# Kernel tuning notes

Hardware: AMD Instinct MI355X
Metric: run time of the kernel (lower is better)

Reference implementation:

```python
import jax, jax.numpy as jnp
import numpy as np

R = 32            # voxel resolution
ALPHA = 0.1       # LeakyReLU slope
BN_EPS = 1e-4     # BatchNormalization epsilon
VOX_EPS = 1e-6    # Voxelization eps (normalize=True)


def _bn_train(x, gamma, beta, axes):
    # training-mode batch norm over `axes`, channel axis = 1
    mean = jnp.mean(x, axes, keepdims=True)
    var = jnp.var(x, axes, keepdims=True)
    bshape = (1, -1) + (1,) * (x.ndim - 2)
    return gamma.reshape(bshape) * (x - mean) * jax.lax.rsqrt(var + BN_EPS) + beta.reshape(bshape)


def _lrelu(x):
    return jnp.where(x >= 0, x, ALPHA * x)


def _voxelize(features, coords):
    # features [B,C,N], coords [B,3,N] -> grid [B,C,R,R,R], norm_coords [B,3,N] in [0,R-1]
    centered = coords - jnp.mean(coords, axis=2, keepdims=True)
    max_norm = jnp.max(jnp.linalg.norm(centered, axis=1, keepdims=True), axis=2, keepdims=True)
    norm = centered / (max_norm * 2.0 + VOX_EPS) + 0.5
    norm = jnp.clip(norm * R, 0.0, R - 1)
    vox = jnp.round(norm).astype(jnp.int32)              # [B,3,N]
    flat = (vox[:, 0] * R + vox[:, 1]) * R + vox[:, 2]   # [B,N]

    def per_batch(f, idx):  # f [C,N], idx [N]
        sums = jax.ops.segment_sum(f.T, idx, num_segments=R ** 3)            # [R^3,C]
        cnt = jax.ops.segment_sum(jnp.ones_like(idx, f.dtype), idx, num_segments=R ** 3)
        return (sums / jnp.maximum(cnt, 1.0)[:, None]).T                      # [C,R^3]

    grid = jax.vmap(per_batch)(features, flat)            # [B,C,R^3]
    B, C = features.shape[0], features.shape[1]
    return grid.reshape(B, C, R, R, R), norm


def _conv3d(x, w, b):
    # x [B,C,D,H,W], w [k,k,k,Cin,Cout], 'same' padding
    y = jax.lax.conv_general_dilated(x, w, (1, 1, 1), 'SAME',
                                     dimension_numbers=('NCDHW', 'DHWIO', 'NCDHW'))
    return y + b.reshape(1, -1, 1, 1, 1)


def _trilinear_devoxelize(vf, coords):
    # vf [B,C,R^3], coords [B,3,N] in [0,R-1] -> [B,C,N]
    c0f = jnp.clip(jnp.floor(coords), 0.0, R - 1)
    frac = coords - c0f                                   # [B,3,N]
    c0 = c0f.astype(jnp.int32)
    c1 = jnp.minimum(c0 + 1, R - 1)
    out = jnp.zeros((vf.shape[0], vf.shape[1], coords.shape[2]), vf.dtype)
    for dx in (0, 1):
        for dy in (0, 1):
            for dz in (0, 1):
                xs = c1[:, 0] if dx else c0[:, 0]
                ys = c1[:, 1] if dy else c0[:, 1]
                zs = c1[:, 2] if dz else c0[:, 2]
                w = ((frac[:, 0] if dx else 1 - frac[:, 0]) *
                     (frac[:, 1] if dy else 1 - frac[:, 1]) *
                     (frac[:, 2] if dz else 1 - frac[:, 2]))           # [B,N]
                idx = (xs * R + ys) * R + zs                            # [B,N]
                g = jnp.take_along_axis(vf, idx[:, None, :], axis=2)    # [B,C,N]
                out = out + w[:, None, :] * g
    return out


def setup_inputs() -> dict:
    key = jax.random.key(0)
    ks = jax.random.split(key, 16)
    B, C, N, K = 8, 64, 16384, 3
    s = 0.05
    return {
        'features': jax.random.normal(ks[0], (B, C, N), jnp.float32),
        'coords': jax.random.normal(ks[1], (B, 3, N), jnp.float32),
        'conv1_w': jax.random.normal(ks[2], (K, K, K, C, C), jnp.float32) * s,
        'conv1_b': jnp.zeros((C,), jnp.float32),
        'bn1_gamma': jnp.ones((C,), jnp.float32),
        'bn1_beta': jnp.zeros((C,), jnp.float32),
        'conv2_w': jax.random.normal(ks[3], (K, K, K, C, C), jnp.float32) * s,
        'conv2_b': jnp.zeros((C,), jnp.float32),
        'bn2_gamma': jnp.ones((C,), jnp.float32),
        'bn2_beta': jnp.zeros((C,), jnp.float32),
        'pf_w': jax.random.normal(ks[4], (C, C), jnp.float32) * s,
        'pf_bias': jnp.zeros((C,), jnp.float32),
        'pf_gamma': jnp.ones((C,), jnp.float32),
        'pf_beta': jnp.zeros((C,), jnp.float32),
    }


def reference(features, coords, conv1_w, conv1_b, bn1_gamma, bn1_beta,
              conv2_w, conv2_b, bn2_gamma, bn2_beta,
              pf_w, pf_bias, pf_gamma, pf_beta):
    vgrid, norm_coords = _voxelize(features, coords)
    v = _lrelu(_bn_train(_conv3d(vgrid, conv1_w, conv1_b), bn1_gamma, bn1_beta, (0, 2, 3, 4)))
    v = _lrelu(_bn_train(_conv3d(v, conv2_w, conv2_b), bn2_gamma, bn2_beta, (0, 2, 3, 4)))
    vflat = v.reshape(v.shape[0], v.shape[1], -1)                 # [B,C,R^3]
    vpts = _trilinear_devoxelize(vflat, norm_coords)              # [B,C,N]
    # point branch: shared MLP (1x1 conv) + BN + LeakyReLU
    p = jnp.einsum('bcn,cd->bdn', features, pf_w) + pf_bias[None, :, None]
    p = _lrelu(_bn_train(p, pf_gamma, pf_beta, (0, 2)))
    return vpts + p, coords
```

## Files before the change

kernel.cpp:

```cpp
#include <hip/hip_runtime.h>
#include <stdint.h>

#define RR 32
#define R3 32768
#define NB 8
#define NCH 64
#define NP 16384

typedef unsigned short u16;
typedef uint32_t u32;
typedef __attribute__((ext_vector_type(8))) short bf8;
typedef __attribute__((ext_vector_type(4))) float f4;
typedef __attribute__((ext_vector_type(16))) float f16x;

#define MFMA(a,b,c)   __builtin_amdgcn_mfma_f32_16x16x32_bf16(a,b,c,0,0,0)
#define MFMA32(a,b,c) __builtin_amdgcn_mfma_f32_32x32x16_bf16(a,b,c,0,0,0)

__device__ __forceinline__ float bf2f(u16 v){
  union { u32 u; float f; } x; x.u = ((u32)v) << 16; return x.f;
}
__device__ __forceinline__ float u2f(u32 u){
  union { u32 u; float f; } x; x.u = u; return x.f;
}
__device__ __forceinline__ u16 f2bf(float f){
  union { float f; u32 u; } x; x.f = f;
  u32 r = x.u + 0x7fffu + ((x.u >> 16) & 1u);
  return (u16)(r >> 16);
}
__device__ __forceinline__ float ldf(const void* p, size_t i, int isbf){
  return isbf ? bf2f(((const u16*)p)[i]) : ((const float*)p)[i];
}

#define OFF_GRID  0ull
#define OFF_BUF1  33554432ull
#define OFF_FT    33554432ull
#define OFF_P     67108864ull
#define OFF_CNT   83886080ull
#define OFF_SMALL 84934656ull
#define OFF_STAT  84936704ull
#define OFF_OFFS  84948992ull
#define OFF_NC    85997568ull
#define OFF_VIDX  87570432ull
#define OFF_SORT  88094720ull
#define OFF_WF1   88619008ull
#define OFF_WF2   88840192ull
#define OFF_WFP   89061376ull
#define WS_NEED   89069568ull
#define ZOFF      OFF_CNT
#define ZBYTES    1062912ull

__global__ void k_dtype(const uint32_t* __restrict__ gamma_raw, int* __restrict__ flag){
  if (threadIdx.x == 0) *flag = (gamma_raw[0] == 0x3F800000u) ? 0 : 1;
}

__global__ void k_coordstats(const void* __restrict__ coords, float* __restrict__ small,
                             const int* __restrict__ dflag){
  int b = blockIdx.x; int tid = threadIdx.x;
  int isbf = *dflag;
  __shared__ float red[1024];
  size_t cb = (size_t)b*3*NP;
  float sx=0.f, sy=0.f, sz=0.f;
  for (int n = tid; n < NP; n += 1024){
    sx += ldf(coords, cb+n, isbf);
    sy += ldf(coords, cb+NP+n, isbf);
    sz += ldf(coords, cb+2*NP+n, isbf);
  }
  float m[3]; float* sums[3] = {&sx,&sy,&sz};
  for (int a = 0; a < 3; a++){
    red[tid] = *sums[a]; __syncthreads();
    for (int s = 512; s > 0; s >>= 1){ if (tid < s) red[tid] += red[tid+s]; __syncthreads(); }
    m[a] = red[0] * (1.0f/NP); __syncthreads();
  }
  float vm = 0.f;
  for (int n = tid; n < NP; n += 1024){
    float cx = ldf(coords, cb+n, isbf)      - m[0];
    float cy = ldf(coords, cb+NP+n, isbf)   - m[1];
    float cz = ldf(coords, cb+2*NP+n, isbf) - m[2];
    vm = fmaxf(vm, sqrtf(cx*cx + cy*cy + cz*cz));
  }
  red[tid] = vm; __syncthreads();
  for (int s = 512; s > 0; s >>= 1){ if (tid < s) red[tid] = fmaxf(red[tid], red[tid+s]); __syncthreads(); }
  if (tid == 0){
    small[384 + b*4 + 0] = m[0];
    small[384 + b*4 + 1] = m[1];
    small[384 + b*4 + 2] = m[2];
    small[384 + b*4 + 3] = 1.0f / (2.0f*red[0] + 1e-6f);
  }
}

__global__ void k_pointprep(const void* __restrict__ coords, const float* __restrict__ small,
                            float* __restrict__ nc, int* __restrict__ vidx, int* __restrict__ cnt,
                            const int* __restrict__ dflag){
  int g = blockIdx.x*256 + threadIdx.x;
  int isbf = *dflag;
  int b = g >> 14; int n = g & (NP-1);
  float mx = small[384+b*4+0], my = small[384+b*4+1], mz = small[384+b*4+2], sc = small[384+b*4+3];
  size_t cb = (size_t)b*3*NP;
  float nx = ((ldf(coords, cb+n, isbf)      - mx)*sc + 0.5f) * 32.0f;
  float ny = ((ldf(coords, cb+NP+n, isbf)   - my)*sc + 0.5f) * 32.0f;
  float nz = ((ldf(coords, cb+2*NP+n, isbf) - mz)*sc + 0.5f) * 32.0f;
  nx = fminf(fmaxf(nx, 0.f), 31.f);
  ny = fminf(fmaxf(ny, 0.f), 31.f);
  nz = fminf(fmaxf(nz, 0.f), 31.f);
  nc[(b*3+0)*NP + n] = nx; nc[(b*3+1)*NP + n] = ny; nc[(b*3+2)*NP + n] = nz;
  int vx = (int)rintf(nx), vy = (int)rintf(ny), vz = (int)rintf(nz);
  int flat = (vx*32 + vy)*32 + vz;
  vidx[g] = flat;
  atomicAdd(&cnt[b*R3 + flat], 1);
}

__global__ void k_scan(const int* __restrict__ cnt, int* __restrict__ off){
  __shared__ int part[1024];
  int b = blockIdx.x, tid = threadIdx.x;
  int base = b*R3 + tid*32;
  int s = 0;
  for (int i = 0; i < 32; i++) s += cnt[base + i];
  part[tid] = s; __syncthreads();
  for (int st = 1; st < 1024; st <<= 1){
    int v = (tid >= st) ? part[tid - st] : 0;
    __syncthreads();
    part[tid] += v;
    __syncthreads();
  }
  int run = (tid == 0) ? 0 : part[tid - 1];
  for (int i = 0; i < 32; i++){ off[base + i] = run; run += cnt[base + i]; }
}

__global__ void k_sortpts(const int* __restrict__ vidx, int* __restrict__ off, int* __restrict__ sorted){
  int g = blockIdx.x*256 + threadIdx.x;
  int b = g >> 14; int n = g & (NP-1);
  int v = vidx[g];
  int slot = atomicAdd(&off[b*R3 + v], 1);
  sorted[b*NP + slot] = n;
}

__global__ __launch_bounds__(256) void k_voxsum(const u16* __restrict__ fT, const int* __restrict__ sorted,
                         const int* __restrict__ cnt, const int* __restrict__ off,
                         u16* __restrict__ grid){
  int wid = blockIdx.x*4 + (threadIdx.x >> 6);
  int lane = threadIdx.x & 63;
  int b = wid >> 11;
  int v0 = (wid & 2047) << 4;
  int base = b*R3 + v0;
  int c = 0, e = 0;
  if (lane < 16){ c = cnt[base + lane]; e = off[base + lane]; }
  int start = __shfl(e - c, 0);
  int total = __shfl(e, 15) - start;
  const int* sb = sorted + (size_t)b*NP;
  int sp = 0;
  if (lane < total) sp = sb[start + lane];
  #pragma unroll
  for (int i = 0; i < 16; i++){
    int ci = __shfl(c, i);
    int rel = __shfl(e, i) - ci - start;
    float a0 = 0.f, a1 = 0.f;
    int j = 0;
    for (; j + 1 < ci; j += 2){
      int k0 = rel + j, k1 = k0 + 1;
      int n0 = (k0 < 64) ? __shfl(sp, k0) : sb[start + k0];
      int n1 = (k1 < 64) ? __shfl(sp, k1) : sb[start + k1];
      a0 += bf2f(fT[((size_t)(b*NP + n0))*64 + lane]);
      a1 += bf2f(fT[((size_t)(b*NP + n1))*64 + lane]);
    }
    if (j < ci){
      int k0 = rel + j;
      int n0 = (k0 < 64) ? __shfl(sp, k0) : sb[start + k0];
      a0 += bf2f(fT[((size_t)(b*NP + n0))*64 + lane]);
    }
    float acc = a0 + a1;
    grid[((size_t)(base + i))*64 + lane] = f2bf(acc / (float)max(ci, 1));
  }
}

__global__ void k_wprep(const void* __restrict__ w, u16* __restrict__ wfrag, const int* __restrict__ dflag){
  int idx = blockIdx.x; int lane = threadIdx.x;
  int isbf = *dflag;
  int ntl = idx & 3; int kk = (idx >> 2) & 1; int tap = idx >> 3;
  int lh = lane & 15, quad = lane >> 4;
  int n = ntl*16 + lh;
  u16* dst = wfrag + ((size_t)idx*64 + lane)*8;
  for (int j = 0; j < 8; j++){
    int k = kk*32 + quad*8 + j;
    dst[j] = f2bf(ldf(w, (size_t)(tap*64 + k)*64 + n, isbf));
  }
}

__global__ void k_wprep32(const void* __restrict__ w, u16* __restrict__ wfrag, const int* __restrict__ dflag){
  int idx = blockIdx.x; int lane = threadIdx.x;
  int isbf = *dflag;
  int nh = idx & 1; int ks = (idx >> 1) & 3; int tap = idx >> 3;
  int n = nh*32 + (lane & 31);
  int khalf = lane >> 5;
  u16* dst = wfrag + ((size_t)idx*64 + lane)*8;
  for (int j = 0; j < 8; j++){
    int cin = ks*16 + khalf*8 + j;
    dst[j] = f2bf(ldf(w, (size_t)(tap*64 + cin)*64 + n, isbf));
  }
}

__device__ __forceinline__ void bn_params(const float* __restrict__ spread, int c, float invM,
                                          float* mean, float* rs){
  float su = 0.f, sq = 0.f;
  #pragma unroll
  for (int i = 0; i < 8; i++){ su += spread[i*128 + c]; sq += spread[i*128 + 64 + c]; }
  float m = su * invM;
  *mean = m;
  *rs = rsqrtf(sq*invM - m*m + 1e-4f);
}

#define ISSUE_W8(BANK, TAP) do { \
  _Pragma("unroll") \
  for (int k_ = 0; k_ < 8; k_++) \
    BANK[k_] = *(const bf8*)(wstream + (size_t)((TAP)*8 + k_)*512); \
} while(0)

#define ISSUE_A4(B0, TAP) do { \
  const int t_ = (TAP); \
  const int dwi_ = t_ % 3, dvi_ = (t_/3) % 3, dui_ = t_/9; \
  const u16* rp_ = &lds_in[((dui_ + usel)*4 + vsel + dvi_)*2176]; \
  const int wp_ = mlane + dwi_; \
  const int wb_ = wp_*64, wx_ = wp_ & 7; \
  _Pragma("unroll") \
  for (int ks_ = 0; ks_ < 4; ks_++){ \
    const int off_ = wb_ + ((((ks_*2) + khalf) ^ wx_) << 3); \
    B0[ks_] = *(const bf8*)(rp_ + off_); \
  } \
} while(0)

#define CONSUME(BW, B0) do { \
  _Pragma("unroll") \
  for (int ks_ = 0; ks_ < 4; ks_++){ \
    acc0 = MFMA32(B0[ks_], BW[ks_*2+0], acc0); \
    acc1 = MFMA32(B0[ks_], BW[ks_*2+1], acc1); \
  } \
} while(0)

template<int BN>
__global__ __launch_bounds__(256, 2) void k_conv_t(const u16* __restrict__ in, const u16* __restrict__ wfrag,
                                                   u16* __restrict__ out, const float* __restrict__ spread,
                                                   const void* __restrict__ gamma, const void* __restrict__ beta,
                                                   const int* __restrict__ dflag){
  __shared__ u16 lds_in[16*2176];
  __shared__ float bnA[64], bnB[64];
  int bx = blockIdx.x;
  int b = bx >> 8; int r = bx & 255;
  int u0 = (r >> 4) * 2; int v0 = (r & 15) * 2;
  int tid = threadIdx.x, wv = tid >> 6, lane = tid & 63;

  if constexpr (BN){
    if (tid < 64){
      int isbf = *dflag;
      float mean, rs;
      bn_params(spread, tid, 1.0f/(NB*R3), &mean, &rs);
      float ga = ldf(gamma, tid, isbf), be = ldf(beta, tid, isbf);
      float A = ga*rs;
      bnA[tid] = A; bnB[tid] = be - mean*A;
    }
    __syncthreads();
  }

  uint4 zz; zz.x = 0; zz.y = 0; zz.z = 0; zz.w = 0;
  for (int ri = wv; ri < 16; ri += 4){
    int u2 = u0 + (ri >> 2) - 1;
    int v2 = v0 + (ri & 3) - 1;
    uint4* dstrow = (uint4*)&lds_in[ri*2176];
    if ((unsigned)u2 > 31u || (unsigned)v2 > 31u){
      for (int i = lane; i < 272; i += 64) dstrow[i] = zz;
      continue;
    }
    const uint4* src = (const uint4*)(in + ((size_t)(b*R3 + (u2*32 + v2)*32))*64);
    if (lane < 8) dstrow[lane] = zz;
    else if (lane < 16) dstrow[264 + (lane & 7)] = zz;
    #pragma unroll
    for (int ch = 0; ch < 4; ch++){
      int idx = ch*64 + lane;
      int w = idx >> 3, cc = idx & 7;
      uint4 v = src[idx];
      if constexpr (BN){
        u32 in4[4] = {v.x, v.y, v.z, v.w};
        u32 o4[4];
        #pragma unroll
        for (int k = 0; k < 4; k++){
          int c = cc*8 + 2*k;
          float lo = u2f(in4[k] << 16);
          float hi = u2f(in4[k] & 0xFFFF0000u);
          lo = bnA[c]*lo + bnB[c];     lo = (lo >= 0.f) ? lo : 0.1f*lo;
          hi = bnA[c+1]*hi + bnB[c+1]; hi = (hi >= 0.f) ? hi : 0.1f*hi;
          o4[k] = (u32)f2bf(lo) | ((u32)f2bf(hi) << 16);
        }
        v.x = o4[0]; v.y = o4[1]; v.z = o4[2]; v.w = o4[3];
      }
      int wp = w + 1;
      dstrow[wp*8 + (cc ^ (wp & 7))] = v;
    }
  }
  __syncthreads();

  int usel = wv >> 1, vsel = wv & 1;
  int u_i = u0 + usel, v_i = v0 + vsel;
  int mlane = lane & 31;
  int khalf = lane >> 5;
  f16x acc0, acc1;
  #pragma unroll
  for (int i = 0; i < 16; i++){ acc0[i] = 0.f; acc1[i] = 0.f; }

  const u16* wstream = wfrag + (size_t)lane*8;

  bf8 W0[8], W1[8], W2[8];
  bf8 Aa[4], Ab[4];

  ISSUE_W8(W0, 0);
  ISSUE_W8(W1, 1);
  ISSUE_A4(Aa, 0);

  #pragma unroll
  for (int tap = 0; tap < 27; ++tap){
    const int pf = tap + 2;
    if (pf < 27){
      if (pf % 3 == 0)      ISSUE_W8(W0, pf);
      else if (pf % 3 == 1) ISSUE_W8(W1, pf);
      else                  ISSUE_W8(W2, pf);
    }
    if (tap + 1 < 27){
      if ((tap + 1) & 1) ISSUE_A4(Ab, tap + 1);
      else               ISSUE_A4(Aa, tap + 1);
    }
    __builtin_amdgcn_sched_barrier(0);
    if (tap < 25)       asm volatile("s_waitcnt vmcnt(16) lgkmcnt(4)");
    else if (tap == 25) asm volatile("s_waitcnt vmcnt(8) lgkmcnt(4)");
    else                asm volatile("s_waitcnt vmcnt(0) lgkmcnt(0)");
    __builtin_amdgcn_sched_barrier(0);
    const int wsel = tap % 3, asel = tap & 1;
    if (wsel == 0){ if (asel == 0) CONSUME(W0, Aa); else CONSUME(W0, Ab); }
    else if (wsel == 1){ if (asel == 0) CONSUME(W1, Aa); else CONSUME(W1, Ab); }
    else              { if (asel == 0) CONSUME(W2, Aa); else CONSUME(W2, Ab); }
  }

  int rbase = 4*khalf;
  size_t base0 = ((size_t)(b*R3 + (u_i*32 + v_i)*32))*64;
  #pragma unroll
  for (int reg = 0; reg < 16; reg++){
    int row = (reg & 3) + 8*(reg >> 2) + rbase;
    out[base0 + (size_t)row*64 + mlane]      = f2bf(acc0[reg]);
    out[base0 + (size_t)row*64 + 32 + mlane] = f2bf(acc1[reg]);
  }
}

__global__ __launch_bounds__(256) void k_stats2(const u16* __restrict__ buf, float* __restrict__ spread, int M){
  __shared__ float sred[4*128];
  int tid = threadIdx.x, bx = blockIdx.x;
  int wv = tid >> 6, lane = tid & 63;
  int sub = lane & 7;
  int g = bx*256 + tid;
  float s[8], s2[8];
  #pragma unroll
  for (int j = 0; j < 8; j++){ s[j] = 0.f; s2[j] = 0.f; }
  const uint4* p4 = (const uint4*)buf;
  size_t total = (size_t)M * 8;
  for (size_t f = g; f < total; f += 262144){
    uint4 v = p4[f];
    u32 ws_[4] = {v.x, v.y, v.z, v.w};
    #pragma unroll
    for (int k = 0; k < 4; k++){
      float lo = u2f(ws_[k] << 16);
      float hi = u2f(ws_[k] & 0xFFFF0000u);
      s[2*k]   += lo; s2[2*k]   += lo*lo;
      s[2*k+1] += hi; s2[2*k+1] += hi*hi;
    }
  }
  #pragma unroll
  for (int j = 0; j < 8; j++){
    #pragma unroll
    for (int m = 8; m <= 32; m <<= 1){
      s[j]  += __shfl_xor(s[j],  m);
      s2[j] += __shfl_xor(s2[j], m);
    }
  }
  if (lane < 8){
    #pragma unroll
    for (int j = 0; j < 8; j++){
      sred[wv*128 + sub*8 + j]      = s[j];
      sred[wv*128 + 64 + sub*8 + j] = s2[j];
    }
  }
  __syncthreads();
  if (tid < 128){
    float t = sred[tid] + sred[128+tid] + sred[256+tid] + sred[384+tid];
    atomicAdd(&spread[(bx & 7)*128 + tid], t);
  }
}

__global__ void k_ftrans(const void* __restrict__ feat, u16* __restrict__ fT, const int* __restrict__ dflag){
  __shared__ u16 t[64*65];
  int bx = blockIdx.x;
  int isbf = *dflag;
  int b = bx >> 8; int n0 = (bx & 255) * 64;
  int tid = threadIdx.x;
  int nl = tid & 63; int cq = tid >> 6;
  for (int cp = 0; cp < 16; cp++){
    int c = cq + cp*4;
    t[c*65 + nl] = f2bf(ldf(feat, ((size_t)(b*NCH + c))*NP + n0 + nl, isbf));
  }
  __syncthreads();
  for (int np2 = 0; np2 < 16; np2++){
    int n = np2*4 + cq; int c = nl;
    fT[((size_t)(b*NP + n0 + n))*64 + c] = t[c*65 + n];
  }
}

__global__ void k_pgemm(const u16* __restrict__ fT, const u16* __restrict__ wfp, u16* __restrict__ p){
  __shared__ u16 As[128*64];
  int bx = blockIdx.x;
  size_t row0 = (size_t)bx * 128;
  int tid = threadIdx.x, wv = tid >> 6, lane = tid & 63;
  const uint4* src = (const uint4*)(fT + row0*64);
  uint4* dst = (uint4*)As;
  for (int i = tid; i < 1024; i += 256) dst[i] = src[i];
  __syncthreads();
  int lh = lane & 15, quad = lane >> 4;
  f4 z4 = {0.f,0.f,0.f,0.f};
  f4 acc[2][4];
  for (int i = 0; i < 2; i++) for (int j = 0; j < 4; j++) acc[i][j] = z4;
  const u16* ap = &As[(wv*32)*64];
  #pragma unroll
  for (int kk = 0; kk < 2; kk++){
    bf8 a0 = *(const bf8*)(ap + lh*64 + kk*32 + quad*8);
    bf8 a1 = *(const bf8*)(ap + (16+lh)*64 + kk*32 + quad*8);
    #pragma unroll
    for (int ntl = 0; ntl < 4; ntl++){
      bf8 bf = *(const bf8*)(wfp + ((size_t)(kk*4 + ntl)*64 + lane)*8);
      acc[0][ntl] = MFMA(a0, bf, acc[0][ntl]);
      acc[1][ntl] = MFMA(a1, bf, acc[1][ntl]);
    }
  }
  #pragma unroll
  for (int mt = 0; mt < 2; mt++)
    for (int ntl = 0; ntl < 4; ntl++)
      for (int reg = 0; reg < 4; reg++){
        int rr = wv*32 + mt*16 + quad*4 + reg;
        p[(row0 + rr)*64 + ntl*16 + lh] = f2bf(acc[mt][ntl][reg]);
      }
}

__global__ void k_devox(const u16* __restrict__ grid, const u16* __restrict__ p,
                        const float* __restrict__ stP, const float* __restrict__ st2,
                        const void* __restrict__ pfg, const void* __restrict__ pfb,
                        const void* __restrict__ g2, const void* __restrict__ b2,
                        const float* __restrict__ nc, void* __restrict__ out0,
                        const int* __restrict__ dflag){
  __shared__ float t[64*65];
  int bx = blockIdx.x;
  int isbf = *dflag;
  int b = bx >> 8; int n0 = (bx & 255) * 64;
  int tid = threadIdx.x, wv = tid >> 6, lane = tid & 63;
  int c = lane;
  float meanP, rsP;
  bn_params(stP, c, 1.0f/(NB*NP), &meanP, &rsP);
  float gaP = ldf(pfg, c, isbf), beP = ldf(pfb, c, isbf);
  float mean2, rs2;
  bn_params(st2, c, 1.0f/(NB*R3), &mean2, &rs2);
  float ga2 = ldf(g2, c, isbf), be2 = ldf(b2, c, isbf);
  float A2 = ga2*rs2, B2 = be2 - mean2*A2;
  for (int pt = wv; pt < 64; pt += 4){
    int n = n0 + pt;
    float nx = nc[(b*3+0)*NP + n];
    float ny = nc[(b*3+1)*NP + n];
    float nz = nc[(b*3+2)*NP + n];
    float x0f = floorf(nx), y0f = floorf(ny), z0f = floorf(nz);
    int x0 = (int)x0f, y0 = (int)y0f, z0 = (int)z0f;
    float fx = nx - x0f, fy = ny - y0f, fz = nz - z0f;
    int x1 = min(x0+1,31), y1 = min(y0+1,31), z1 = min(z0+1,31);
    float acc = 0.f;
    #pragma unroll
    for (int k = 0; k < 8; k++){
      int dx = k >> 2, dy = (k >> 1) & 1, dz = k & 1;
      int xs = dx ? x1 : x0, ys = dy ? y1 : y0, zs = dz ? z1 : z0;
      float wgt = (dx ? fx : 1.f-fx)*(dy ? fy : 1.f-fy)*(dz ? fz : 1.f-fz);
      float gv = bf2f(grid[((size_t)(b*R3 + (xs*32+ys)*32 + zs))*64 + c]);
      gv = A2*gv + B2;
      gv = (gv >= 0.f) ? gv : 0.1f*gv;
      acc += wgt * gv;
    }
    float pv = bf2f(p[((size_t)(b*NP + n))*64 + c]);
    float y = gaP*(pv - meanP)*rsP + beP;
    y = (y >= 0.f) ? y : 0.1f*y;
    t[pt*65 + c] = acc + y;
  }
  __syncthreads();
  for (int cp = 0; cp < 16; cp++){
    int co = wv + cp*4;
    size_t oi = ((size_t)(b*NCH + co))*NP + n0 + lane;
    float val = t[lane*65 + co];
    if (isbf) ((u16*)out0)[oi] = f2bf(val);
    else      ((float*)out0)[oi] = val;
  }
}

__global__ void k_copycoords(const void* __restrict__ coords, void* __restrict__ out0,
                             const int* __restrict__ dflag){
  int g = blockIdx.x*256 + threadIdx.x;
  int isbf = *dflag;
  size_t oi = (size_t)NB*NCH*NP + g;
  if (isbf) ((u16*)out0)[oi]   = ((const u16*)coords)[g];
  else      ((float*)out0)[oi] = ((const float*)coords)[g];
}

extern "C" void kernel_launch(void* const* d_in, const int* in_sizes, int n_in,
                              void* d_out, int out_size, void* d_ws, size_t ws_size,
                              hipStream_t stream){
  if (ws_size < WS_NEED) return;

  const void* feat   = d_in[0];
  const void* coords = d_in[1];
  const void* w1     = d_in[2];
  const void* g1     = d_in[4];
  const void* b1     = d_in[5];
  const void* w2     = d_in[6];
  const void* g2     = d_in[8];
  const void* b2     = d_in[9];
  const void* pw     = d_in[10];
  const void* pg     = d_in[12];
  const void* pb     = d_in[13];

  char* ws = (char*)d_ws;
  u16*   gridv = (u16*)(ws + OFF_GRID);
  u16*   buf1  = (u16*)(ws + OFF_BUF1);
  u16*   fT    = (u16*)(ws + OFF_FT);
  u16*   p     = (u16*)(ws + OFF_P);
  int*   cnt   = (int*)(ws + OFF_CNT);
  float* small = (float*)(ws + OFF_SMALL);
  int*   dflag = (int*)(small + 448);
  float* stat  = (float*)(ws + OFF_STAT);
  int*   offs  = (int*)(ws + OFF_OFFS);
  float* nc    = (float*)(ws + OFF_NC);
  int*   vidx  = (int*)(ws + OFF_VIDX);
  int*   sorted= (int*)(ws + OFF_SORT);
  u16*   wf1   = (u16*)(ws + OFF_WF1);
  u16*   wf2   = (u16*)(ws + OFF_WF2);
  u16*   wfp   = (u16*)(ws + OFF_WFP);

  hipMemsetAsync(ws + ZOFF, 0, ZBYTES, stream);
  k_dtype<<<1, 64, 0, stream>>>((const uint32_t*)g1, dflag);

  k_wprep32<<<27*8, 64, 0, stream>>>(w1, wf1, dflag);
  k_wprep32<<<27*8, 64, 0, stream>>>(w2, wf2, dflag);
  k_wprep<<<8, 64, 0, stream>>>(pw, wfp, dflag);

  k_coordstats<<<NB, 1024, 0, stream>>>(coords, small, dflag);
  k_pointprep<<<NB*NP/256, 256, 0, stream>>>(coords, small, nc, vidx, cnt, dflag);
  k_scan<<<NB, 1024, 0, stream>>>(cnt, offs);
  k_sortpts<<<NB*NP/256, 256, 0, stream>>>(vidx, offs, sorted);

  k_ftrans<<<NB*NP/64, 256, 0, stream>>>(feat, fT, dflag);
  k_voxsum<<<NB*R3/64, 256, 0, stream>>>(fT, sorted, cnt, offs, gridv);
  k_pgemm<<<NB*NP/128, 256, 0, stream>>>(fT, wfp, p);
  k_stats2<<<1024, 256, 0, stream>>>(p, stat + 2048, NB*NP);

  k_conv_t<0><<<NB*256, 256, 0, stream>>>(gridv, wf1, buf1, nullptr, nullptr, nullptr, nullptr);
  k_stats2<<<1024, 256, 0, stream>>>(buf1, stat + 0, NB*R3);

  k_conv_t<1><<<NB*256, 256, 0, stream>>>(buf1, wf2, gridv, stat + 0, g1, b1, dflag);
  k_stats2<<<1024, 256, 0, stream>>>(gridv, stat + 1024, NB*R3);

  k_devox<<<NB*NP/64, 256, 0, stream>>>(gridv, p, stat + 2048, stat + 1024,
                                        pg, pb, g2, b2, nc, d_out, dflag);
  k_copycoords<<<NB*3*NP/256, 256, 0, stream>>>(coords, d_out, dflag);
}
```

Measured before the change: 421.4 us.

## Enlarge conv3d tile to 4x4 rows per block with 2 rows per wave

Each conv block now covers a 4x4 set of (u,v) rows using 8 waves, and each wave computes two u-rows. Every weight fragment loaded from global memory therefore feeds twice as many MFMAs, and the halo overhead in LDS shrinks from 16 staged rows per 4 outputs to 36 per 16. The cost is higher register pressure (four 16-float accumulators plus doubled A fragments), a larger LDS footprint (about 157 KB), and only 512 blocks total, which may reduce occupancy.

```diff
diff --git a/kernel.cpp b/kernel.cpp
--- a/kernel.cpp
+++ b/kernel.cpp
@@ -210,41 +210,45 @@
 
 #define ISSUE_W8(BANK, TAP) do { \
   _Pragma("unroll") \
-  for (int k_ = 0; k_ < 8; k_++) \
-    BANK[k_] = *(const bf8*)(wstream + (size_t)((TAP)*8 + k_)*512); \
+  for (int f_ = 0; f_ < 8; f_++) \
+    BANK[f_] = *(const bf8*)(wstream + (size_t)((TAP)*8 + f_)*512); \
 } while(0)
 
-#define ISSUE_A4(B0, TAP) do { \
+#define ISSUE_A8(BANK, TAP) do { \
   const int t_ = (TAP); \
   const int dwi_ = t_ % 3, dvi_ = (t_/3) % 3, dui_ = t_/9; \
-  const u16* rp_ = &lds_in[((dui_ + usel)*4 + vsel + dvi_)*2176]; \
+  const u16* rp0_ = &lds_in[((2*uhalf + dui_)*6 + vsel + dvi_)*2176]; \
+  const u16* rp1_ = rp0_ + 6*2176; \
   const int wp_ = mlane + dwi_; \
   const int wb_ = wp_*64, wx_ = wp_ & 7; \
   _Pragma("unroll") \
   for (int ks_ = 0; ks_ < 4; ks_++){ \
     const int off_ = wb_ + ((((ks_*2) + khalf) ^ wx_) << 3); \
-    B0[ks_] = *(const bf8*)(rp_ + off_); \
+    BANK[ks_]     = *(const bf8*)(rp0_ + off_); \
+    BANK[4 + ks_] = *(const bf8*)(rp1_ + off_); \
   } \
 } while(0)
 
-#define CONSUME(BW, B0) do { \
+#define CONSUME16(BW, BA) do { \
   _Pragma("unroll") \
   for (int ks_ = 0; ks_ < 4; ks_++){ \
-    acc0 = MFMA32(B0[ks_], BW[ks_*2+0], acc0); \
-    acc1 = MFMA32(B0[ks_], BW[ks_*2+1], acc1); \
+    acc00 = MFMA32(BA[ks_],     BW[ks_*2+0], acc00); \
+    acc01 = MFMA32(BA[ks_],     BW[ks_*2+1], acc01); \
+    acc10 = MFMA32(BA[4 + ks_], BW[ks_*2+0], acc10); \
+    acc11 = MFMA32(BA[4 + ks_], BW[ks_*2+1], acc11); \
   } \
 } while(0)
 
 template<int BN>
-__global__ __launch_bounds__(256, 2) void k_conv_t(const u16* __restrict__ in, const u16* __restrict__ wfrag,
+__global__ __launch_bounds__(512, 2) void k_conv_t(const u16* __restrict__ in, const u16* __restrict__ wfrag,
                                                    u16* __restrict__ out, const float* __restrict__ spread,
                                                    const void* __restrict__ gamma, const void* __restrict__ beta,
                                                    const int* __restrict__ dflag){
-  __shared__ u16 lds_in[16*2176];
+  __shared__ u16 lds_in[36*2176];
   __shared__ float bnA[64], bnB[64];
   int bx = blockIdx.x;
-  int b = bx >> 8; int r = bx & 255;
-  int u0 = (r >> 4) * 2; int v0 = (r & 15) * 2;
+  int b = bx >> 6; int r = bx & 63;
+  int u0 = (r >> 3) * 4; int v0 = (r & 7) * 4;
   int tid = threadIdx.x, wv = tid >> 6, lane = tid & 63;
 
   if constexpr (BN){
@@ -260,9 +264,9 @@
   }
 
   uint4 zz; zz.x = 0; zz.y = 0; zz.z = 0; zz.w = 0;
-  for (int ri = wv; ri < 16; ri += 4){
-    int u2 = u0 + (ri >> 2) - 1;
-    int v2 = v0 + (ri & 3) - 1;
+  for (int ri = wv; ri < 36; ri += 8){
+    int u2 = u0 + (ri / 6) - 1;
+    int v2 = v0 + (ri % 6) - 1;
     uint4* dstrow = (uint4*)&lds_in[ri*2176];
     if ((unsigned)u2 > 31u || (unsigned)v2 > 31u){
       for (int i = lane; i < 272; i += 64) dstrow[i] = zz;
@@ -296,22 +300,22 @@
   }
   __syncthreads();
 
-  int usel = wv >> 1, vsel = wv & 1;
-  int u_i = u0 + usel, v_i = v0 + vsel;
+  int vsel = wv & 3, uhalf = wv >> 2;
+  int v_i = v0 + vsel;
   int mlane = lane & 31;
   int khalf = lane >> 5;
-  f16x acc0, acc1;
-  #pragma unroll
-  for (int i = 0; i < 16; i++){ acc0[i] = 0.f; acc1[i] = 0.f; }
+  f16x acc00, acc01, acc10, acc11;
+  #pragma unroll
+  for (int i = 0; i < 16; i++){ acc00[i] = 0.f; acc01[i] = 0.f; acc10[i] = 0.f; acc11[i] = 0.f; }
 
   const u16* wstream = wfrag + (size_t)lane*8;
 
   bf8 W0[8], W1[8], W2[8];
-  bf8 Aa[4], Ab[4];
+  bf8 Aa[8], Ab[8];
 
   ISSUE_W8(W0, 0);
   ISSUE_W8(W1, 1);
-  ISSUE_A4(Aa, 0);
+  ISSUE_A8(Aa, 0);
 
   #pragma unroll
   for (int tap = 0; tap < 27; ++tap){
@@ -322,27 +326,30 @@
       else                  ISSUE_W8(W2, pf);
     }
     if (tap + 1 < 27){
-      if ((tap + 1) & 1) ISSUE_A4(Ab, tap + 1);
-      else               ISSUE_A4(Aa, tap + 1);
+      if ((tap + 1) & 1) ISSUE_A8(Ab, tap + 1);
+      else               ISSUE_A8(Aa, tap + 1);
     }
     __builtin_amdgcn_sched_barrier(0);
-    if (tap < 25)       asm volatile("s_waitcnt vmcnt(16) lgkmcnt(4)");
-    else if (tap == 25) asm volatile("s_waitcnt vmcnt(8) lgkmcnt(4)");
+    if (tap < 25)       asm volatile("s_waitcnt vmcnt(16) lgkmcnt(8)");
+    else if (tap == 25) asm volatile("s_waitcnt vmcnt(8) lgkmcnt(8)");
     else                asm volatile("s_waitcnt vmcnt(0) lgkmcnt(0)");
     __builtin_amdgcn_sched_barrier(0);
     const int wsel = tap % 3, asel = tap & 1;
-    if (wsel == 0){ if (asel == 0) CONSUME(W0, Aa); else CONSUME(W0, Ab); }
-    else if (wsel == 1){ if (asel == 0) CONSUME(W1, Aa); else CONSUME(W1, Ab); }
-    else              { if (asel == 0) CONSUME(W2, Aa); else CONSUME(W2, Ab); }
+    if (wsel == 0){ if (asel == 0) CONSUME16(W0, Aa); else CONSUME16(W0, Ab); }
+    else if (wsel == 1){ if (asel == 0) CONSUME16(W1, Aa); else CONSUME16(W1, Ab); }
+    else              { if (asel == 0) CONSUME16(W2, Aa); else CONSUME16(W2, Ab); }
   }
 
   int rbase = 4*khalf;
-  size_t base0 = ((size_t)(b*R3 + (u_i*32 + v_i)*32))*64;
+  size_t base0 = ((size_t)(b*R3 + ((u0 + 2*uhalf + 0)*32 + v_i)*32))*64;
+  size_t base1 = ((size_t)(b*R3 + ((u0 + 2*uhalf + 1)*32 + v_i)*32))*64;
   #pragma unroll
   for (int reg = 0; reg < 16; reg++){
     int row = (reg & 3) + 8*(reg >> 2) + rbase;
-    out[base0 + (size_t)row*64 + mlane]      = f2bf(acc0[reg]);
-    out[base0 + (size_t)row*64 + 32 + mlane] = f2bf(acc1[reg]);
+    out[base0 + (size_t)row*64 + mlane]      = f2bf(acc00[reg]);
+    out[base0 + (size_t)row*64 + 32 + mlane] = f2bf(acc01[reg]);
+    out[base1 + (size_t)row*64 + mlane]      = f2bf(acc10[reg]);
+    out[base1 + (size_t)row*64 + 32 + mlane] = f2bf(acc11[reg]);
   }
 }
 
@@ -556,10 +563,10 @@
   k_pgemm<<<NB*NP/128, 256, 0, stream>>>(fT, wfp, p);
   k_stats2<<<1024, 256, 0, stream>>>(p, stat + 2048, NB*NP);
 
-  k_conv_t<0><<<NB*256, 256, 0, stream>>>(gridv, wf1, buf1, nullptr, nullptr, nullptr, nullptr);
+  k_conv_t<0><<<NB*64, 512, 0, stream>>>(gridv, wf1, buf1, nullptr, nullptr, nullptr, nullptr);
   k_stats2<<<1024, 256, 0, stream>>>(buf1, stat + 0, NB*R3);
 
-  k_conv_t<1><<<NB*256, 256, 0, stream>>>(buf1, wf2, gridv, stat + 0, g1, b1, dflag);
+  k_conv_t<1><<<NB*64, 512, 0, stream>>>(buf1, wf2, gridv, stat + 0, g1, b1, dflag);
   k_stats2<<<1024, 256, 0, stream>>>(gridv, stat + 1024, NB*R3);
 
   k_devox<<<NB*NP/64, 256, 0, stream>>>(gridv, p, stat + 2048, stat + 1024,
```

Result: no change. 427.5 us (+1.4%).
